# Optimization experiments

Hardware: AMD Instinct MI355X
Metric: run time of the kernel (lower is better)

Reference implementation:

```python
import jax, jax.numpy as jnp
import numpy as np

N = 100000                       # all_nodes_num
COUNTS = (40000, 30000, 30000)   # node_type_split_list; type 0 is the attributed type
HID = 64                         # args.hidden_dim
K = 8                            # args.cluster_num
E = 1_600_000                    # number of edges in g
D_IN = 512                       # in_dims[valid_attributed_type]
NCLS = 16                        # num_classes


def _spmm_mean(h, src, dst):
    """Degree-normalized sparse adjacency @ h via gather/segment_sum (edge-list spmm)."""
    deg = jax.ops.segment_sum(jnp.ones_like(src, dtype=h.dtype), dst, num_segments=N)
    agg = jax.ops.segment_sum(h[src], dst, num_segments=N)  # [N, HID]
    return agg / jnp.maximum(deg, 1.0)[:, None]


def setup_inputs() -> dict:
    key = jax.random.key(0)
    ks = jax.random.split(key, 16)
    s = lambda k, shp, fan: jax.random.normal(k, shp, jnp.float32) * np.float32(1.0 / np.sqrt(fan))
    return {
        "feats0": jax.random.normal(ks[0], (COUNTS[0], D_IN), jnp.float32),
        "W_pre": s(ks[1], (D_IN, HID), D_IN), "b_pre": jnp.zeros((HID,), jnp.float32),
        "emb_W": s(ks[2], (2, COUNTS[1], HID), COUNTS[1]), "emb_b": jnp.zeros((2, HID), jnp.float32),
        "op_W": s(ks[3], (K, HID, HID), HID), "op_b": jnp.zeros((K, HID), jnp.float32),
        "fc_W": s(ks[4], (2, HID, HID), HID), "fc_b": jnp.zeros((2, HID), jnp.float32),
        "gnn_W": s(ks[5], (HID, HID), HID), "gnn_b": jnp.zeros((HID,), jnp.float32),
        "out_W": s(ks[6], (HID, NCLS), HID), "out_b": jnp.zeros((NCLS,), jnp.float32),
        "src": jax.random.randint(ks[7], (E,), 0, N, jnp.int32),
        "dst": jax.random.randint(ks[8], (E,), 0, N, jnp.int32),
        "node_assign": jax.random.randint(ks[9], (N,), 0, K, jnp.int32),
    }


def reference(feats0, W_pre, b_pre, emb_W, emb_b, op_W, op_b, fc_W, fc_b,
              gnn_W, gnn_b, out_W, out_b, src, dst, node_assign):
    # preprocess: Linear on the attributed type, scattered into h0 over all nodes
    h_attr = feats0 @ W_pre + b_pre                       # [n0, HID]
    h0 = jnp.zeros((N, HID), feats0.dtype).at[:COUNTS[0]].set(h_attr)

    # 'one-hot' embeddings: Linear applied to sparse identity == weight rows + bias
    one_hot_h = jnp.concatenate([
        jnp.zeros((COUNTS[0], HID), feats0.dtype),
        emb_W[0] + emb_b[0],
        emb_W[1] + emb_b[1],
    ], axis=0)                                            # [N, HID]

    # shared heterogeneous-graph aggregation (edge-list spmm), per-cluster op linear,
    # then diagonal cluster mask (spmm with diagonal selection matrix == row masking)
    agg = _spmm_mean(h0, src, dst)                        # [N, HID]
    h_att = h0
    for k in range(K):
        mask = (node_assign == k)[:, None]
        gcn_k = agg @ op_W[k] + op_b[k]                   # per-cluster GNN op output
        h_att = h_att + jnp.where(mask, gcn_k + one_hot_h, 0.0)

    # useTypeLinear: per-type Linear for non-attributed types, identity for attributed
    parts = [h_att[:COUNTS[0]]]
    off = COUNTS[0]
    for i in range(2):
        seg = h_att[off:off + COUNTS[1 + i]]
        parts.append(seg @ fc_W[i] + fc_b[i])
        off += COUNTS[1 + i]
    h_t = jnp.concatenate(parts, axis=0)                  # [N, HID]

    # downstream GCN-style model: spmm -> linear -> elu, then classifier head
    node_emb = jax.nn.elu(_spmm_mean(h_t, src, dst) @ gnn_W + gnn_b)
    logits = node_emb @ out_W + out_b
    return node_emb, logits, logits
```

## Files before the change

### kernel.cpp

```cpp
#include <hip/hip_runtime.h>
#include <hip/hip_bf16.h>

#define NN   100000
#define C0   40000
#define C1   30000
#define C2   30000
#define HID  64
#define KK   8
#define EE   1600000
#define DIN  512
#define NCLS 16
#define NB   196
#define BKE  2048
#define GR1  782
#define NBC  1568
#define MAXT 1571
#define FCT  469
#define GNT  1563
#define AP   88

typedef unsigned short ushortT;
typedef __attribute__((ext_vector_type(8))) short bf16x8;
typedef __attribute__((ext_vector_type(4))) float f32x4;

__device__ __forceinline__ float b2f(ushortT u) {
    return __uint_as_float((unsigned)u << 16);
}
__device__ __forceinline__ ushortT f2b(float x) {
    unsigned v = __float_as_uint(x);
    unsigned r = (v + 0x7FFF + ((v >> 16) & 1)) >> 16;
    return (ushortT)r;
}
__device__ __forceinline__ unsigned pk2(float lo, float hi) {
    return (unsigned)f2b(lo) | ((unsigned)f2b(hi) << 16);
}
__device__ __forceinline__ void acc8f(float* a, uint4 v) {
    a[0] += b2f((ushortT)(v.x & 0xFFFF)); a[1] += b2f((ushortT)(v.x >> 16));
    a[2] += b2f((ushortT)(v.y & 0xFFFF)); a[3] += b2f((ushortT)(v.y >> 16));
    a[4] += b2f((ushortT)(v.z & 0xFFFF)); a[5] += b2f((ushortT)(v.z >> 16));
    a[6] += b2f((ushortT)(v.w & 0xFFFF)); a[7] += b2f((ushortT)(v.w >> 16));
}

__global__ __launch_bounds__(256) void setup_k(const int* __restrict__ dst,
                                               const int* __restrict__ na,
                                               const float* __restrict__ W,
                                               int* __restrict__ bcnt,
                                               int* __restrict__ nbc,
                                               ushortT* __restrict__ WT) {
    __shared__ int sh[NB];
    const int t = threadIdx.x, b = blockIdx.x;
    if (b < GR1) {
        for (int i = t; i < NB; i += 256) sh[i] = 0;
        __syncthreads();
        const int base = b * BKE;
        for (int u = 0; u < BKE / 256; ++u) {
            int e = base + t + u * 256;
            if (e < EE) atomicAdd(&sh[dst[e] >> 9], 1);
        }
        __syncthreads();
        for (int i = t; i < NB; i += 256) {
            int c = sh[i];
            if (c) atomicAdd(&bcnt[i], c);
        }
    } else if (b < GR1 + NB) {
        const int nb_ = b - GR1;
        if (t < KK) sh[t] = 0;
        __syncthreads();
        #pragma unroll
        for (int u = 0; u < 2; ++u) {
            int n = nb_ * 512 + t + u * 256;
            if (n < NN) atomicAdd(&sh[na[n]], 1);
        }
        __syncthreads();
        if (t < KK) nbc[t * NB + nb_] = sh[t];
    } else {
        int idx = (b - GR1 - NB) * 256 + t;
        int c = idx >> 6, k8 = (idx & 63) * 8;
        uint4 v;
        v.x = pk2(W[(size_t)(k8 + 0) * HID + c], W[(size_t)(k8 + 1) * HID + c]);
        v.y = pk2(W[(size_t)(k8 + 2) * HID + c], W[(size_t)(k8 + 3) * HID + c]);
        v.z = pk2(W[(size_t)(k8 + 4) * HID + c], W[(size_t)(k8 + 5) * HID + c]);
        v.w = pk2(W[(size_t)(k8 + 6) * HID + c], W[(size_t)(k8 + 7) * HID + c]);
        *(uint4*)(WT + (size_t)c * DIN + k8) = v;
    }
}

__global__ __launch_bounds__(256) void pre_mfma(const float* __restrict__ A,
                                                const ushortT* __restrict__ WT,
                                                const float* __restrict__ b,
                                                ushortT* __restrict__ hb) {
    __shared__ ushortT Ak[2][64 * AP];
    __shared__ ushortT Bk[2][64 * AP];
    const int tid = threadIdx.x;
    const int row0 = blockIdx.x * 64;
    const int rr = tid >> 2, q = tid & 3;
    const int w = tid >> 6, l = tid & 63;
    const int lr = l & 15, g = l >> 4;
    f32x4 acc[4] = {{0.f,0.f,0.f,0.f},{0.f,0.f,0.f,0.f},{0.f,0.f,0.f,0.f},{0.f,0.f,0.f,0.f}};
    float4 av0, av1, av2, av3;
    uint4 bv0, bv1;
    {
        const float* ap = A + (size_t)(row0 + rr) * DIN + q * 16;
        av0 = *(const float4*)(ap + 0);  av1 = *(const float4*)(ap + 4);
        av2 = *(const float4*)(ap + 8);  av3 = *(const float4*)(ap + 12);
        const uint4* bp = (const uint4*)(WT + (size_t)rr * DIN + q * 16);
        bv0 = bp[0]; bv1 = bp[1];
    }
    {
        uint4 ua0, ua1;
        ua0.x = pk2(av0.x, av0.y); ua0.y = pk2(av0.z, av0.w);
        ua0.z = pk2(av1.x, av1.y); ua0.w = pk2(av1.z, av1.w);
        ua1.x = pk2(av2.x, av2.y); ua1.y = pk2(av2.z, av2.w);
        ua1.z = pk2(av3.x, av3.y); ua1.w = pk2(av3.z, av3.w);
        *(uint4*)&Ak[0][rr * AP + q * 16] = ua0;
        *(uint4*)&Ak[0][rr * AP + q * 16 + 8] = ua1;
        *(uint4*)&Bk[0][rr * AP + q * 16] = bv0;
        *(uint4*)&Bk[0][rr * AP + q * 16 + 8] = bv1;
    }
    __syncthreads();
    for (int t = 0; t < 8; ++t) {
        if (t < 7) {
            const int k0 = (t + 1) * 64;
            const float* ap = A + (size_t)(row0 + rr) * DIN + k0 + q * 16;
            av0 = *(const float4*)(ap + 0);  av1 = *(const float4*)(ap + 4);
            av2 = *(const float4*)(ap + 8);  av3 = *(const float4*)(ap + 12);
            const uint4* bp = (const uint4*)(WT + (size_t)rr * DIN + k0 + q * 16);
            bv0 = bp[0]; bv1 = bp[1];
        }
        const int bu = t & 1;
        #pragma unroll
        for (int s = 0; s < 2; ++s) {
            bf16x8 af = *(const bf16x8*)&Ak[bu][(w * 16 + lr) * AP + s * 32 + g * 8];
            #pragma unroll
            for (int n = 0; n < 4; ++n) {
                bf16x8 bf = *(const bf16x8*)&Bk[bu][(n * 16 + lr) * AP + s * 32 + g * 8];
                acc[n] = __builtin_amdgcn_mfma_f32_16x16x32_bf16(af, bf, acc[n], 0, 0, 0);
            }
        }
        if (t < 7) {
            const int nb = (t + 1) & 1;
            uint4 ua0, ua1;
            ua0.x = pk2(av0.x, av0.y); ua0.y = pk2(av0.z, av0.w);
            ua0.z = pk2(av1.x, av1.y); ua0.w = pk2(av1.z, av1.w);
            ua1.x = pk2(av2.x, av2.y); ua1.y = pk2(av2.z, av2.w);
            ua1.z = pk2(av3.x, av3.y); ua1.w = pk2(av3.z, av3.w);
            *(uint4*)&Ak[nb][rr * AP + q * 16] = ua0;
            *(uint4*)&Ak[nb][rr * AP + q * 16 + 8] = ua1;
            *(uint4*)&Bk[nb][rr * AP + q * 16] = bv0;
            *(uint4*)&Bk[nb][rr * AP + q * 16 + 8] = bv1;
        }
        __syncthreads();
    }
    #pragma unroll
    for (int n = 0; n < 4; ++n) {
        float bb = b[n * 16 + lr];
        #pragma unroll
        for (int i = 0; i < 4; ++i) {
            int row = row0 + w * 16 + g * 4 + i;
            hb[(size_t)row * HID + n * 16 + lr] = f2b(acc[n][i] + bb);
        }
    }
}

__global__ __launch_bounds__(256) void scan_k(const int* __restrict__ bcnt,
                                              int* __restrict__ bbase,
                                              int* __restrict__ bcur,
                                              int* __restrict__ offs,
                                              const int* __restrict__ nbc,
                                              int* __restrict__ gbase,
                                              int* __restrict__ koff,
                                              int* __restrict__ tmap_b,
                                              int* __restrict__ tmap_s) {
    const int t = threadIdx.x;
    if (blockIdx.x == 0) {
        if (t == 0) {
            int run = 0;
            for (int i = 0; i < NB; ++i) { bbase[i] = run; bcur[i] = run; run += bcnt[i]; }
            offs[NN] = EE;
        }
        return;
    }
    __shared__ int sm[256];
    __shared__ int carry;
    __shared__ int tl[KK];
    if (t == 0) carry = 0;
    for (int i = t; i < MAXT; i += 256) tmap_b[i] = -1;
    __syncthreads();
    for (int c = 0; c < 7; ++c) {
        int i = c * 256 + t;
        int v = (i < NBC) ? nbc[i] : 0;
        sm[t] = v;
        __syncthreads();
        for (int off = 1; off < 256; off <<= 1) {
            int y = (t >= off) ? sm[t - off] : 0;
            __syncthreads();
            sm[t] += y;
            __syncthreads();
        }
        int base = carry;
        int excl = base + sm[t] - v;
        if (i < NBC) {
            gbase[i] = excl;
            if ((i % NB) == 0) koff[i / NB] = excl;
        }
        __syncthreads();
        if (t == 255) carry = base + sm[255];
        __syncthreads();
    }
    if (t == 0) {
        koff[KK] = NN;
        int run = 0;
        for (int k = 0; k < KK; ++k) {
            tl[k] = run;
            int cnt = ((k == KK - 1) ? NN : koff[k + 1]) - koff[k];
            run += (cnt + 63) / 64;
        }
    }
    __syncthreads();
    if (t < KK) {
        int k = t;
        int kb = koff[k];
        int ke = (k == KK - 1) ? NN : koff[k + 1];
        int nt = (ke - kb + 63) / 64;
        for (int tt = 0; tt < nt; ++tt) {
            tmap_b[tl[k] + tt] = k;
            tmap_s[tl[k] + tt] = kb + tt * 64;
        }
    }
}

__global__ __launch_bounds__(256) void scatter_k(const int* __restrict__ src,
                                                 const int* __restrict__ dst,
                                                 int* __restrict__ bcur,
                                                 unsigned* __restrict__ ebuf,
                                                 const int* __restrict__ na,
                                                 const int* __restrict__ gbase,
                                                 int* __restrict__ perm) {
    __shared__ int s1[NB];
    __shared__ int s2[NB];
    const int t = threadIdx.x, b = blockIdx.x;
    if (b < GR1) {
        for (int i = t; i < NB; i += 256) s1[i] = 0;
        __syncthreads();
        const int base = b * BKE;
        unsigned mypk[8]; int mybin[8], myrank[8];
        #pragma unroll
        for (int u = 0; u < 8; ++u) {
            int e = base + t + u * 256;
            if (e < EE) {
                int d = dst[e];
                int s = src[e];
                mybin[u] = d >> 9;
                mypk[u] = (unsigned)s |
                          ((unsigned)(((d & 511) << 1) | (s < C0 ? 0 : 1)) << 17);
                myrank[u] = atomicAdd(&s1[mybin[u]], 1);
            } else mybin[u] = -1;
        }
        __syncthreads();
        for (int i = t; i < NB; i += 256) {
            int c = s1[i];
            s2[i] = c ? atomicAdd(&bcur[i], c) : 0;
        }
        __syncthreads();
        #pragma unroll
        for (int u = 0; u < 8; ++u) {
            if (mybin[u] >= 0) {
                ebuf[s2[mybin[u]] + myrank[u]] = mypk[u];
            }
        }
    } else {
        const int nb_ = b - GR1;
        if (t < KK) { s1[t] = 0; s2[t] = gbase[t * NB + nb_]; }
        __syncthreads();
        #pragma unroll
        for (int u = 0; u < 2; ++u) {
            int n = nb_ * 512 + t + u * 256;
            if (n < NN) {
                int k = na[n];
                int r = atomicAdd(&s1[k], 1);
                perm[s2[k] + r] = n;
            }
        }
    }
}

__global__ __launch_bounds__(256) void fine_scatter(const unsigned* __restrict__ ebuf,
                                                    const int* __restrict__ bbase,
                                                    const int* __restrict__ bend,
                                                    int* __restrict__ offs,
                                                    int* __restrict__ split,
                                                    int* __restrict__ ssrc) {
    __shared__ int hist[1024];
    __shared__ int lofs[1024];
    __shared__ int sm[256];
    const int t = threadIdx.x, b = blockIdx.x;
    const int beg = bbase[b], end = bend[b];
    for (int i = t; i < 1024; i += 256) hist[i] = 0;
    __syncthreads();
    for (int j = beg + t; j < end; j += 256) {
        unsigned pk = ebuf[j];
        atomicAdd(&hist[pk >> 17], 1);
    }
    __syncthreads();
    int v0 = hist[4 * t], v1 = hist[4 * t + 1], v2 = hist[4 * t + 2], v3 = hist[4 * t + 3];
    int ts = v0 + v1 + v2 + v3;
    sm[t] = ts;
    __syncthreads();
    for (int off = 1; off < 256; off <<= 1) {
        int y = (t >= off) ? sm[t - off] : 0;
        __syncthreads();
        sm[t] += y;
        __syncthreads();
    }
    int pre = sm[t] - ts;
    lofs[4 * t] = pre; lofs[4 * t + 1] = pre + v0;
    lofs[4 * t + 2] = pre + v0 + v1; lofs[4 * t + 3] = pre + v0 + v1 + v2;
    __syncthreads();
    const int d0 = b * 512;
    for (int i = t; i < 512; i += 256) {
        int n = d0 + i;
        if (n < NN) {
            offs[n]  = beg + lofs[2 * i];
            split[n] = beg + lofs[2 * i + 1];
        }
    }
    __syncthreads();
    for (int j = beg + t; j < end; j += 256) {
        unsigned pk = ebuf[j];
        int pos = beg + atomicAdd(&lofs[pk >> 17], 1);
        ssrc[pos] = (int)(pk & 0x1FFFFu);
    }
}

__global__ __launch_bounds__(256) void spmm(const ushortT* __restrict__ rows,
                                            const int* __restrict__ offs,
                                            const int* __restrict__ splt,
                                            const int* __restrict__ ssrc,
                                            ushortT* __restrict__ aggb) {
    const int t = threadIdx.x;
    const int g = t >> 3, c8 = t & 7;
    const int n = blockIdx.x * 32 + g;
    const int beg = offs[n], endf = offs[n + 1];
    const int ge = splt ? splt[n] : endf;
    float a[8] = {}, c[8] = {};
    int j = beg;
    for (; j + 8 <= ge; j += 8) {
        int s0 = ssrc[j + 0], s1 = ssrc[j + 1], s2 = ssrc[j + 2], s3 = ssrc[j + 3];
        int s4 = ssrc[j + 4], s5 = ssrc[j + 5], s6 = ssrc[j + 6], s7 = ssrc[j + 7];
        uint4 v0 = *(const uint4*)(rows + (size_t)s0 * HID + c8 * 8);
        uint4 v1 = *(const uint4*)(rows + (size_t)s1 * HID + c8 * 8);
        uint4 v2 = *(const uint4*)(rows + (size_t)s2 * HID + c8 * 8);
        uint4 v3 = *(const uint4*)(rows + (size_t)s3 * HID + c8 * 8);
        uint4 v4 = *(const uint4*)(rows + (size_t)s4 * HID + c8 * 8);
        uint4 v5 = *(const uint4*)(rows + (size_t)s5 * HID + c8 * 8);
        uint4 v6 = *(const uint4*)(rows + (size_t)s6 * HID + c8 * 8);
        uint4 v7 = *(const uint4*)(rows + (size_t)s7 * HID + c8 * 8);
        acc8f(a, v0); acc8f(c, v1); acc8f(a, v2); acc8f(c, v3);
        acc8f(a, v4); acc8f(c, v5); acc8f(a, v6); acc8f(c, v7);
    }
    if (j + 4 <= ge) {
        int s0 = ssrc[j + 0], s1 = ssrc[j + 1], s2 = ssrc[j + 2], s3 = ssrc[j + 3];
        uint4 v0 = *(const uint4*)(rows + (size_t)s0 * HID + c8 * 8);
        uint4 v1 = *(const uint4*)(rows + (size_t)s1 * HID + c8 * 8);
        uint4 v2 = *(const uint4*)(rows + (size_t)s2 * HID + c8 * 8);
        uint4 v3 = *(const uint4*)(rows + (size_t)s3 * HID + c8 * 8);
        acc8f(a, v0); acc8f(c, v1); acc8f(a, v2); acc8f(c, v3);
        j += 4;
    }
    for (; j < ge; ++j) {
        uint4 v = *(const uint4*)(rows + (size_t)ssrc[j] * HID + c8 * 8);
        acc8f(a, v);
    }
    const float inv = 1.0f / fmaxf((float)(endf - beg), 1.0f);
    #pragma unroll
    for (int i = 0; i < 8; ++i) a[i] = (a[i] + c[i]) * inv;
    uint4 o;
    o.x = pk2(a[0], a[1]); o.y = pk2(a[2], a[3]);
    o.z = pk2(a[4], a[5]); o.w = pk2(a[6], a[7]);
    *(uint4*)(aggb + (size_t)n * HID + c8 * 8) = o;
}

__device__ __forceinline__ void gemm64(const float As[64][65], const float Bs[64][64],
                                       float acc[4][4], int tx, int ty) {
    for (int kk = 0; kk < 64; ++kk) {
        float a0 = As[ty * 4 + 0][kk], a1 = As[ty * 4 + 1][kk];
        float a2 = As[ty * 4 + 2][kk], a3 = As[ty * 4 + 3][kk];
        float4 bv = *(const float4*)(&Bs[kk][tx * 4]);
        acc[0][0] += a0 * bv.x; acc[0][1] += a0 * bv.y; acc[0][2] += a0 * bv.z; acc[0][3] += a0 * bv.w;
        acc[1][0] += a1 * bv.x; acc[1][1] += a1 * bv.y; acc[1][2] += a1 * bv.z; acc[1][3] += a1 * bv.w;
        acc[2][0] += a2 * bv.x; acc[2][1] += a2 * bv.y; acc[2][2] += a2 * bv.z; acc[2][3] += a2 * bv.w;
        acc[3][0] += a3 * bv.x; acc[3][1] += a3 * bv.y; acc[3][2] += a3 * bv.z; acc[3][3] += a3 * bv.w;
    }
}

__global__ __launch_bounds__(256) void op_gemm(const ushortT* __restrict__ aggb,
                                               const ushortT* __restrict__ hb,
                                               const int* __restrict__ perm,
                                               const int* __restrict__ koff,
                                               const int* __restrict__ tmap_b,
                                               const int* __restrict__ tmap_s,
                                               const float* __restrict__ op_W,
                                               const float* __restrict__ op_b,
                                               const float* __restrict__ emb_W,
                                               const float* __restrict__ emb_b,
                                               ushortT* __restrict__ htb) {
    __shared__ float As[64][65];
    __shared__ float Bs[64][64];
    __shared__ int idx[64];
    const int bk = tmap_b[blockIdx.x];
    if (bk < 0) return;
    const int start = tmap_s[blockIdx.x];
    const int kend = koff[bk + 1];
    const int tid = threadIdx.x;
    if (tid < 64) {
        int p = start + tid;
        idx[tid] = (p < kend) ? perm[p] : -1;
    }
    __syncthreads();
    for (int i = tid; i < 64 * 16; i += 256) {
        int r = i >> 4, c4 = i & 15;
        int n = idx[r];
        if (n >= 0) {
            ushort4 u = *(const ushort4*)(aggb + (size_t)n * HID + c4 * 4);
            As[r][c4 * 4 + 0] = b2f(u.x); As[r][c4 * 4 + 1] = b2f(u.y);
            As[r][c4 * 4 + 2] = b2f(u.z); As[r][c4 * 4 + 3] = b2f(u.w);
        } else {
            As[r][c4 * 4 + 0] = 0.f; As[r][c4 * 4 + 1] = 0.f;
            As[r][c4 * 4 + 2] = 0.f; As[r][c4 * 4 + 3] = 0.f;
        }
    }
    for (int i = tid; i < 64 * 16; i += 256) {
        int r = i >> 4, c4 = i & 15;
        *(float4*)(&Bs[r][c4 * 4]) = *(const float4*)(op_W + (size_t)bk * HID * HID + (size_t)r * HID + c4 * 4);
    }
    __syncthreads();
    const int tx = tid & 15, ty = tid >> 4;
    float acc[4][4] = {};
    gemm64(As, Bs, acc, tx, ty);
    float4 ob = *(const float4*)(op_b + (size_t)bk * HID + tx * 4);
    #pragma unroll
    for (int rr = 0; rr < 4; ++rr) {
        int n = idx[ty * 4 + rr];
        if (n < 0) continue;
        float4 v;
        v.x = acc[rr][0] + ob.x; v.y = acc[rr][1] + ob.y;
        v.z = acc[rr][2] + ob.z; v.w = acc[rr][3] + ob.w;
        if (n < C0) {
            ushort4 hu = *(const ushort4*)(hb + (size_t)n * HID + tx * 4);
            v.x += b2f(hu.x); v.y += b2f(hu.y); v.z += b2f(hu.z); v.w += b2f(hu.w);
        } else {
            int si = (n < C0 + C1) ? 0 : 1;
            int rn = n - C0 - si * C1;
            float4 ew = *(const float4*)(emb_W + ((size_t)si * C1 + rn) * HID + tx * 4);
            float4 eb = *(const float4*)(emb_b + (size_t)si * HID + tx * 4);
            v.x += ew.x + eb.x; v.y += ew.y + eb.y;
            v.z += ew.z + eb.z; v.w += ew.w + eb.w;
        }
        ushort4 o;
        o.x = f2b(v.x); o.y = f2b(v.y); o.z = f2b(v.z); o.w = f2b(v.w);
        *(ushort4*)(htb + (size_t)n * HID + tx * 4) = o;
    }
}

__global__ __launch_bounds__(256) void fc_gemm(ushortT* __restrict__ htb,
                                               const float* __restrict__ fc_W,
                                               const float* __restrict__ fc_b) {
    __shared__ float As[64][65];
    __shared__ float Bs[64][64];
    const int si = (blockIdx.x < FCT) ? 0 : 1;
    const int t0 = blockIdx.x - si * FCT;
    const int row0 = C0 + si * C1 + t0 * 64;
    const int lim = C0 + (si + 1) * C1;
    const int tid = threadIdx.x;
    for (int i = tid; i < 64 * 16; i += 256) {
        int r = i >> 4, c4 = i & 15;
        int n = row0 + r;
        if (n < lim) {
            ushort4 u = *(const ushort4*)(htb + (size_t)n * HID + c4 * 4);
            As[r][c4 * 4 + 0] = b2f(u.x); As[r][c4 * 4 + 1] = b2f(u.y);
            As[r][c4 * 4 + 2] = b2f(u.z); As[r][c4 * 4 + 3] = b2f(u.w);
        } else {
            As[r][c4 * 4 + 0] = 0.f; As[r][c4 * 4 + 1] = 0.f;
            As[r][c4 * 4 + 2] = 0.f; As[r][c4 * 4 + 3] = 0.f;
        }
    }
    for (int i = tid; i < 64 * 16; i += 256) {
        int r = i >> 4, c4 = i & 15;
        *(float4*)(&Bs[r][c4 * 4]) = *(const float4*)(fc_W + (size_t)si * HID * HID + (size_t)r * HID + c4 * 4);
    }
    __syncthreads();
    const int tx = tid & 15, ty = tid >> 4;
    float acc[4][4] = {};
    gemm64(As, Bs, acc, tx, ty);
    float4 fb = *(const float4*)(fc_b + (size_t)si * HID + tx * 4);
    #pragma unroll
    for (int rr = 0; rr < 4; ++rr) {
        int n = row0 + ty * 4 + rr;
        if (n >= lim) continue;
        ushort4 o;
        o.x = f2b(acc[rr][0] + fb.x); o.y = f2b(acc[rr][1] + fb.y);
        o.z = f2b(acc[rr][2] + fb.z); o.w = f2b(acc[rr][3] + fb.w);
        *(ushort4*)(htb + (size_t)n * HID + tx * 4) = o;
    }
}

__global__ __launch_bounds__(256) void gnn_logits(const ushortT* __restrict__ aggb,
                                                  const float* __restrict__ gnn_W,
                                                  const float* __restrict__ gnn_b,
                                                  const float* __restrict__ out_W,
                                                  const float* __restrict__ out_b,
                                                  float* __restrict__ out) {
    __shared__ float As[64][65];
    __shared__ float Bs[64][64];
    __shared__ float Wo[64 * NCLS];
    const int row0 = blockIdx.x * 64;
    const int tid = threadIdx.x;
    for (int i = tid; i < 64 * 16; i += 256) {
        int r = i >> 4, c4 = i & 15;
        int n = row0 + r;
        if (n < NN) {
            ushort4 u = *(const ushort4*)(aggb + (size_t)n * HID + c4 * 4);
            As[r][c4 * 4 + 0] = b2f(u.x); As[r][c4 * 4 + 1] = b2f(u.y);
            As[r][c4 * 4 + 2] = b2f(u.z); As[r][c4 * 4 + 3] = b2f(u.w);
        } else {
            As[r][c4 * 4 + 0] = 0.f; As[r][c4 * 4 + 1] = 0.f;
            As[r][c4 * 4 + 2] = 0.f; As[r][c4 * 4 + 3] = 0.f;
        }
    }
    for (int i = tid; i < 64 * 16; i += 256) {
        int r = i >> 4, c4 = i & 15;
        *(float4*)(&Bs[r][c4 * 4]) = *(const float4*)(gnn_W + (size_t)r * HID + c4 * 4);
    }
    *(float4*)(&Wo[tid * 4]) = *(const float4*)(out_W + tid * 4);
    __syncthreads();
    const int tx = tid & 15, ty = tid >> 4;
    float acc[4][4] = {};
    gemm64(As, Bs, acc, tx, ty);
    __syncthreads();
    float4 gb = *(const float4*)(gnn_b + tx * 4);
    #pragma unroll
    for (int rr = 0; rr < 4; ++rr) {
        int n = row0 + ty * 4 + rr;
        float4 v;
        v.x = acc[rr][0] + gb.x; v.y = acc[rr][1] + gb.y;
        v.z = acc[rr][2] + gb.z; v.w = acc[rr][3] + gb.w;
        v.x = (v.x > 0.f) ? v.x : expm1f(v.x);
        v.y = (v.y > 0.f) ? v.y : expm1f(v.y);
        v.z = (v.z > 0.f) ? v.z : expm1f(v.z);
        v.w = (v.w > 0.f) ? v.w : expm1f(v.w);
        As[ty * 4 + rr][tx * 4 + 0] = v.x; As[ty * 4 + rr][tx * 4 + 1] = v.y;
        As[ty * 4 + rr][tx * 4 + 2] = v.z; As[ty * 4 + rr][tx * 4 + 3] = v.w;
        if (n < NN) *(float4*)(out + (size_t)n * HID + tx * 4) = v;
    }
    __syncthreads();
    const int r = tid >> 2, cq = (tid & 3) * 4;
    float l0 = 0.f, l1 = 0.f, l2 = 0.f, l3 = 0.f;
    #pragma unroll 8
    for (int j = 0; j < 64; ++j) {
        float e = As[r][j];
        float4 w = *(const float4*)(&Wo[j * NCLS + cq]);
        l0 += e * w.x; l1 += e * w.y; l2 += e * w.z; l3 += e * w.w;
    }
    int n = row0 + r;
    if (n < NN) {
        float4 ob = *(const float4*)(out_b + cq);
        float4 lg;
        lg.x = l0 + ob.x; lg.y = l1 + ob.y; lg.z = l2 + ob.z; lg.w = l3 + ob.w;
        const size_t lbase = (size_t)NN * HID;
        *(float4*)(out + lbase + (size_t)n * NCLS + cq) = lg;
        *(float4*)(out + lbase + (size_t)NN * NCLS + (size_t)n * NCLS + cq) = lg;
    }
}

extern "C" void kernel_launch(void* const* d_in, const int* in_sizes, int n_in,
                              void* d_out, int out_size, void* d_ws, size_t ws_size,
                              hipStream_t stream) {
    const float* feats0 = (const float*)d_in[0];
    const float* W_pre  = (const float*)d_in[1];
    const float* b_pre  = (const float*)d_in[2];
    const float* emb_W  = (const float*)d_in[3];
    const float* emb_b  = (const float*)d_in[4];
    const float* op_W   = (const float*)d_in[5];
    const float* op_b   = (const float*)d_in[6];
    const float* fc_W   = (const float*)d_in[7];
    const float* fc_b   = (const float*)d_in[8];
    const float* gnn_W  = (const float*)d_in[9];
    const float* gnn_b  = (const float*)d_in[10];
    const float* out_W  = (const float*)d_in[11];
    const float* out_b  = (const float*)d_in[12];
    const int* src         = (const int*)d_in[13];
    const int* dst         = (const int*)d_in[14];
    const int* node_assign = (const int*)d_in[15];
    float* out = (float*)d_out;

    ushortT* hb  = (ushortT*)d_ws;
    ushortT* htb = hb + (size_t)C0 * HID;
    ushortT* aggb = htb + (size_t)NN * HID;
    unsigned* ebuf = (unsigned*)aggb;
    ushortT* WT = aggb + (size_t)NN * HID;
    int* ssrc   = (int*)(WT + (size_t)HID * DIN);
    int* offs   = ssrc + EE;
    int* split  = offs + NN + 1;
    int* perm   = split + NN;
    int* nbc    = perm + NN;
    int* gbase  = nbc + NBC;
    int* koff   = gbase + NBC;
    int* tmap_b = koff + KK + 1;
    int* tmap_s = tmap_b + MAXT;
    int* bcnt   = tmap_s + MAXT;
    int* bbase  = bcnt + NB;
    int* bcur   = bbase + NB;

    hipMemsetAsync(bcnt, 0, NB * sizeof(int), stream);

    setup_k<<<GR1 + NB + 16, 256, 0, stream>>>(dst, node_assign, W_pre, bcnt, nbc, WT);
    pre_mfma<<<C0 / 64, 256, 0, stream>>>(feats0, WT, b_pre, hb);
    scan_k<<<2, 256, 0, stream>>>(bcnt, bbase, bcur, offs, nbc, gbase, koff, tmap_b, tmap_s);
    scatter_k<<<GR1 + NB, 256, 0, stream>>>(src, dst, bcur, ebuf, node_assign, gbase, perm);
    fine_scatter<<<NB, 256, 0, stream>>>(ebuf, bbase, bcur, offs, split, ssrc);
    spmm<<<NN / 32, 256, 0, stream>>>(hb, offs, split, ssrc, aggb);
    op_gemm<<<MAXT, 256, 0, stream>>>(aggb, hb, perm, koff, tmap_b, tmap_s,
                                      op_W, op_b, emb_W, emb_b, htb);
    fc_gemm<<<2 * FCT, 256, 0, stream>>>(htb, fc_W, fc_b);
    spmm<<<NN / 32, 256, 0, stream>>>(htb, offs, nullptr, ssrc, aggb);
    gnn_logits<<<GNT, 256, 0, stream>>>(aggb, gnn_W, gnn_b, out_W, out_b, out);
}
```

Baseline: 223.2 us.

## Fuse per-type fc linear into cluster op GEMM via type-by-cluster binning

Nodes are now binned by (node type, cluster) into 24 bins instead of 8 clusters, so every 64-row tile in op_gemm holds a single type. For non-attributed types the op GEMM result plus embedding is staged in shared memory and immediately multiplied by the per-type fc weight, which removes the separate fc_gemm kernel and its round-trip of htb through global memory. The bucket-offset scan is also parallelised from a serial single-thread loop to a block scan. In exchange the node scan grows from 7 to 19 chunks, there are more partially filled tiles, and some blocks do a second GEMM.

```diff
diff --git a/kernel.cpp b/kernel.cpp
--- a/kernel.cpp
+++ b/kernel.cpp
@@ -13,9 +13,10 @@
 #define NB   196
 #define BKE  2048
 #define GR1  782
-#define NBC  1568
-#define MAXT 1571
-#define FCT  469
+#define NBS  24
+#define NBC  (NBS*NB)
+#define SCH  19
+#define MAXT 1600
 #define GNT  1563
 #define AP   88
 
@@ -39,6 +40,9 @@
     a[2] += b2f((ushortT)(v.y & 0xFFFF)); a[3] += b2f((ushortT)(v.y >> 16));
     a[4] += b2f((ushortT)(v.z & 0xFFFF)); a[5] += b2f((ushortT)(v.z >> 16));
     a[6] += b2f((ushortT)(v.w & 0xFFFF)); a[7] += b2f((ushortT)(v.w >> 16));
+}
+__device__ __forceinline__ int seg_of(int n) {
+    return (n < C0) ? 0 : ((n < C0 + C1) ? 1 : 2);
 }
 
 __global__ __launch_bounds__(256) void setup_k(const int* __restrict__ dst,
@@ -64,15 +68,15 @@
         }
     } else if (b < GR1 + NB) {
         const int nb_ = b - GR1;
-        if (t < KK) sh[t] = 0;
+        if (t < NBS) sh[t] = 0;
         __syncthreads();
         #pragma unroll
         for (int u = 0; u < 2; ++u) {
             int n = nb_ * 512 + t + u * 256;
-            if (n < NN) atomicAdd(&sh[na[n]], 1);
-        }
-        __syncthreads();
-        if (t < KK) nbc[t * NB + nb_] = sh[t];
+            if (n < NN) atomicAdd(&sh[seg_of(n) * KK + na[n]], 1);
+        }
+        __syncthreads();
+        if (t < NBS) nbc[t * NB + nb_] = sh[t];
     } else {
         int idx = (b - GR1 - NB) * 256 + t;
         int c = idx >> 6, k8 = (idx & 63) * 8;
@@ -171,24 +175,10 @@
                                               int* __restrict__ koff,
                                               int* __restrict__ tmap_b,
                                               int* __restrict__ tmap_s) {
+    __shared__ int sm[256];
     const int t = threadIdx.x;
     if (blockIdx.x == 0) {
-        if (t == 0) {
-            int run = 0;
-            for (int i = 0; i < NB; ++i) { bbase[i] = run; bcur[i] = run; run += bcnt[i]; }
-            offs[NN] = EE;
-        }
-        return;
-    }
-    __shared__ int sm[256];
-    __shared__ int carry;
-    __shared__ int tl[KK];
-    if (t == 0) carry = 0;
-    for (int i = t; i < MAXT; i += 256) tmap_b[i] = -1;
-    __syncthreads();
-    for (int c = 0; c < 7; ++c) {
-        int i = c * 256 + t;
-        int v = (i < NBC) ? nbc[i] : 0;
+        int v = (t < NB) ? bcnt[t] : 0;
         sm[t] = v;
         __syncthreads();
         for (int off = 1; off < 256; off <<= 1) {
@@ -197,6 +187,30 @@
             sm[t] += y;
             __syncthreads();
         }
+        if (t < NB) {
+            int excl = sm[t] - v;
+            bbase[t] = excl;
+            bcur[t] = excl;
+        }
+        if (t == 0) offs[NN] = EE;
+        return;
+    }
+    __shared__ int carry;
+    __shared__ int tl[NBS];
+    if (t == 0) carry = 0;
+    for (int i = t; i < MAXT; i += 256) tmap_b[i] = -1;
+    __syncthreads();
+    for (int c = 0; c < SCH; ++c) {
+        int i = c * 256 + t;
+        int v = (i < NBC) ? nbc[i] : 0;
+        sm[t] = v;
+        __syncthreads();
+        for (int off = 1; off < 256; off <<= 1) {
+            int y = (t >= off) ? sm[t - off] : 0;
+            __syncthreads();
+            sm[t] += y;
+            __syncthreads();
+        }
         int base = carry;
         int excl = base + sm[t] - v;
         if (i < NBC) {
@@ -208,19 +222,19 @@
         __syncthreads();
     }
     if (t == 0) {
-        koff[KK] = NN;
+        koff[NBS] = NN;
         int run = 0;
-        for (int k = 0; k < KK; ++k) {
+        for (int k = 0; k < NBS; ++k) {
             tl[k] = run;
-            int cnt = ((k == KK - 1) ? NN : koff[k + 1]) - koff[k];
+            int cnt = ((k == NBS - 1) ? NN : koff[k + 1]) - koff[k];
             run += (cnt + 63) / 64;
         }
     }
     __syncthreads();
-    if (t < KK) {
+    if (t < NBS) {
         int k = t;
         int kb = koff[k];
-        int ke = (k == KK - 1) ? NN : koff[k + 1];
+        int ke = (k == NBS - 1) ? NN : koff[k + 1];
         int nt = (ke - kb + 63) / 64;
         for (int tt = 0; tt < nt; ++tt) {
             tmap_b[tl[k] + tt] = k;
@@ -270,15 +284,15 @@
         }
     } else {
         const int nb_ = b - GR1;
-        if (t < KK) { s1[t] = 0; s2[t] = gbase[t * NB + nb_]; }
+        if (t < NBS) { s1[t] = 0; s2[t] = gbase[t * NB + nb_]; }
         __syncthreads();
         #pragma unroll
         for (int u = 0; u < 2; ++u) {
             int n = nb_ * 512 + t + u * 256;
             if (n < NN) {
-                int k = na[n];
-                int r = atomicAdd(&s1[k], 1);
-                perm[s2[k] + r] = n;
+                int bin = seg_of(n) * KK + na[n];
+                int r = atomicAdd(&s1[bin], 1);
+                perm[s2[bin] + r] = n;
             }
         }
     }
@@ -403,14 +417,18 @@
                                                const float* __restrict__ op_b,
                                                const float* __restrict__ emb_W,
                                                const float* __restrict__ emb_b,
+                                               const float* __restrict__ fc_W,
+                                               const float* __restrict__ fc_b,
                                                ushortT* __restrict__ htb) {
     __shared__ float As[64][65];
     __shared__ float Bs[64][64];
     __shared__ int idx[64];
-    const int bk = tmap_b[blockIdx.x];
-    if (bk < 0) return;
+    const int bin = tmap_b[blockIdx.x];
+    if (bin < 0) return;
+    const int bk = bin & 7;
+    const int si = bin >> 3;
     const int start = tmap_s[blockIdx.x];
-    const int kend = koff[bk + 1];
+    const int kend = koff[bin + 1];
     const int tid = threadIdx.x;
     if (tid < 64) {
         int p = start + tid;
@@ -438,69 +456,54 @@
     float acc[4][4] = {};
     gemm64(As, Bs, acc, tx, ty);
     float4 ob = *(const float4*)(op_b + (size_t)bk * HID + tx * 4);
-    #pragma unroll
-    for (int rr = 0; rr < 4; ++rr) {
-        int n = idx[ty * 4 + rr];
-        if (n < 0) continue;
-        float4 v;
-        v.x = acc[rr][0] + ob.x; v.y = acc[rr][1] + ob.y;
-        v.z = acc[rr][2] + ob.z; v.w = acc[rr][3] + ob.w;
-        if (n < C0) {
+    if (si == 0) {
+        #pragma unroll
+        for (int rr = 0; rr < 4; ++rr) {
+            int n = idx[ty * 4 + rr];
+            if (n < 0) continue;
             ushort4 hu = *(const ushort4*)(hb + (size_t)n * HID + tx * 4);
-            v.x += b2f(hu.x); v.y += b2f(hu.y); v.z += b2f(hu.z); v.w += b2f(hu.w);
-        } else {
-            int si = (n < C0 + C1) ? 0 : 1;
-            int rn = n - C0 - si * C1;
-            float4 ew = *(const float4*)(emb_W + ((size_t)si * C1 + rn) * HID + tx * 4);
-            float4 eb = *(const float4*)(emb_b + (size_t)si * HID + tx * 4);
-            v.x += ew.x + eb.x; v.y += ew.y + eb.y;
-            v.z += ew.z + eb.z; v.w += ew.w + eb.w;
-        }
-        ushort4 o;
-        o.x = f2b(v.x); o.y = f2b(v.y); o.z = f2b(v.z); o.w = f2b(v.w);
-        *(ushort4*)(htb + (size_t)n * HID + tx * 4) = o;
-    }
-}
-
-__global__ __launch_bounds__(256) void fc_gemm(ushortT* __restrict__ htb,
-                                               const float* __restrict__ fc_W,
-                                               const float* __restrict__ fc_b) {
-    __shared__ float As[64][65];
-    __shared__ float Bs[64][64];
-    const int si = (blockIdx.x < FCT) ? 0 : 1;
-    const int t0 = blockIdx.x - si * FCT;
-    const int row0 = C0 + si * C1 + t0 * 64;
-    const int lim = C0 + (si + 1) * C1;
-    const int tid = threadIdx.x;
-    for (int i = tid; i < 64 * 16; i += 256) {
-        int r = i >> 4, c4 = i & 15;
-        int n = row0 + r;
-        if (n < lim) {
-            ushort4 u = *(const ushort4*)(htb + (size_t)n * HID + c4 * 4);
-            As[r][c4 * 4 + 0] = b2f(u.x); As[r][c4 * 4 + 1] = b2f(u.y);
-            As[r][c4 * 4 + 2] = b2f(u.z); As[r][c4 * 4 + 3] = b2f(u.w);
-        } else {
-            As[r][c4 * 4 + 0] = 0.f; As[r][c4 * 4 + 1] = 0.f;
-            As[r][c4 * 4 + 2] = 0.f; As[r][c4 * 4 + 3] = 0.f;
-        }
-    }
-    for (int i = tid; i < 64 * 16; i += 256) {
-        int r = i >> 4, c4 = i & 15;
-        *(float4*)(&Bs[r][c4 * 4]) = *(const float4*)(fc_W + (size_t)si * HID * HID + (size_t)r * HID + c4 * 4);
-    }
-    __syncthreads();
-    const int tx = tid & 15, ty = tid >> 4;
-    float acc[4][4] = {};
-    gemm64(As, Bs, acc, tx, ty);
-    float4 fb = *(const float4*)(fc_b + (size_t)si * HID + tx * 4);
-    #pragma unroll
-    for (int rr = 0; rr < 4; ++rr) {
-        int n = row0 + ty * 4 + rr;
-        if (n >= lim) continue;
-        ushort4 o;
-        o.x = f2b(acc[rr][0] + fb.x); o.y = f2b(acc[rr][1] + fb.y);
-        o.z = f2b(acc[rr][2] + fb.z); o.w = f2b(acc[rr][3] + fb.w);
-        *(ushort4*)(htb + (size_t)n * HID + tx * 4) = o;
+            ushort4 o;
+            o.x = f2b(acc[rr][0] + ob.x + b2f(hu.x));
+            o.y = f2b(acc[rr][1] + ob.y + b2f(hu.y));
+            o.z = f2b(acc[rr][2] + ob.z + b2f(hu.z));
+            o.w = f2b(acc[rr][3] + ob.w + b2f(hu.w));
+            *(ushort4*)(htb + (size_t)n * HID + tx * 4) = o;
+        }
+    } else {
+        const int ei = si - 1;
+        float4 eb = *(const float4*)(emb_b + (size_t)ei * HID + tx * 4);
+        __syncthreads();
+        #pragma unroll
+        for (int rr = 0; rr < 4; ++rr) {
+            int n = idx[ty * 4 + rr];
+            float4 v;
+            v.x = acc[rr][0] + ob.x + eb.x; v.y = acc[rr][1] + ob.y + eb.y;
+            v.z = acc[rr][2] + ob.z + eb.z; v.w = acc[rr][3] + ob.w + eb.w;
+            if (n >= 0) {
+                int rn = n - C0 - ei * C1;
+                float4 ew = *(const float4*)(emb_W + ((size_t)ei * C1 + rn) * HID + tx * 4);
+                v.x += ew.x; v.y += ew.y; v.z += ew.z; v.w += ew.w;
+            }
+            As[ty * 4 + rr][tx * 4 + 0] = v.x; As[ty * 4 + rr][tx * 4 + 1] = v.y;
+            As[ty * 4 + rr][tx * 4 + 2] = v.z; As[ty * 4 + rr][tx * 4 + 3] = v.w;
+        }
+        for (int i = tid; i < 64 * 16; i += 256) {
+            int r = i >> 4, c4 = i & 15;
+            *(float4*)(&Bs[r][c4 * 4]) = *(const float4*)(fc_W + (size_t)ei * HID * HID + (size_t)r * HID + c4 * 4);
+        }
+        __syncthreads();
+        float acc2[4][4] = {};
+        gemm64(As, Bs, acc2, tx, ty);
+        float4 fb = *(const float4*)(fc_b + (size_t)ei * HID + tx * 4);
+        #pragma unroll
+        for (int rr = 0; rr < 4; ++rr) {
+            int n = idx[ty * 4 + rr];
+            if (n < 0) continue;
+            ushort4 o;
+            o.x = f2b(acc2[rr][0] + fb.x); o.y = f2b(acc2[rr][1] + fb.y);
+            o.z = f2b(acc2[rr][2] + fb.z); o.w = f2b(acc2[rr][3] + fb.w);
+            *(ushort4*)(htb + (size_t)n * HID + tx * 4) = o;
+        }
     }
 }
 
@@ -605,7 +608,7 @@
     int* nbc    = perm + NN;
     int* gbase  = nbc + NBC;
     int* koff   = gbase + NBC;
-    int* tmap_b = koff + KK + 1;
+    int* tmap_b = koff + NBS + 1;
     int* tmap_s = tmap_b + MAXT;
     int* bcnt   = tmap_s + MAXT;
     int* bbase  = bcnt + NB;
@@ -620,8 +623,7 @@
     fine_scatter<<<NB, 256, 0, stream>>>(ebuf, bbase, bcur, offs, split, ssrc);
     spmm<<<NN / 32, 256, 0, stream>>>(hb, offs, split, ssrc, aggb);
     op_gemm<<<MAXT, 256, 0, stream>>>(aggb, hb, perm, koff, tmap_b, tmap_s,
-                                      op_W, op_b, emb_W, emb_b, htb);
-    fc_gemm<<<2 * FCT, 256, 0, stream>>>(htb, fc_W, fc_b);
+                                      op_W, op_b, emb_W, emb_b, fc_W, fc_b, htb);
     spmm<<<NN / 32, 256, 0, stream>>>(htb, offs, nullptr, ssrc, aggb);
     gnn_logits<<<GNT, 256, 0, stream>>>(aggb, gnn_W, gnn_b, out_W, out_b, out);
 }
```

New measurement: 238.6 us. 1.07x slower.

## Fuse histogram setup into the pre-linear MFMA kernel and parallelize bucket scan

Applied to the files above, without the earlier changes.

Moves the dst-bucket histogram and per-cluster node counts out of the setup kernel and into the same launch as the preprocessing MFMA GEMM, as extra blocks that reuse its LDS. A small kernel now does the weight transpose and zeroes the bucket counters, replacing the memset. The serial single-thread bucket prefix sum becomes a 256-thread parallel scan. The goal is to cut launch overhead and let the atomic-heavy histogram overlap with the GEMM, at the cost of mixing heterogeneous blocks in one grid.

```diff
diff --git a/kernel.cpp b/kernel.cpp
--- a/kernel.cpp
+++ b/kernel.cpp
@@ -13,7 +13,9 @@
 #define NB   196
 #define BKE  2048
 #define GR1  782
+#define PMB  625
 #define NBC  1568
+#define SCH  7
 #define MAXT 1571
 #define FCT  469
 #define GNT  1563
@@ -41,40 +43,12 @@
     a[6] += b2f((ushortT)(v.w & 0xFFFF)); a[7] += b2f((ushortT)(v.w >> 16));
 }
 
-__global__ __launch_bounds__(256) void setup_k(const int* __restrict__ dst,
-                                               const int* __restrict__ na,
-                                               const float* __restrict__ W,
-                                               int* __restrict__ bcnt,
-                                               int* __restrict__ nbc,
-                                               ushortT* __restrict__ WT) {
-    __shared__ int sh[NB];
+__global__ __launch_bounds__(256) void zero_wt(const float* __restrict__ W,
+                                               ushortT* __restrict__ WT,
+                                               int* __restrict__ bcnt) {
     const int t = threadIdx.x, b = blockIdx.x;
-    if (b < GR1) {
-        for (int i = t; i < NB; i += 256) sh[i] = 0;
-        __syncthreads();
-        const int base = b * BKE;
-        for (int u = 0; u < BKE / 256; ++u) {
-            int e = base + t + u * 256;
-            if (e < EE) atomicAdd(&sh[dst[e] >> 9], 1);
-        }
-        __syncthreads();
-        for (int i = t; i < NB; i += 256) {
-            int c = sh[i];
-            if (c) atomicAdd(&bcnt[i], c);
-        }
-    } else if (b < GR1 + NB) {
-        const int nb_ = b - GR1;
-        if (t < KK) sh[t] = 0;
-        __syncthreads();
-        #pragma unroll
-        for (int u = 0; u < 2; ++u) {
-            int n = nb_ * 512 + t + u * 256;
-            if (n < NN) atomicAdd(&sh[na[n]], 1);
-        }
-        __syncthreads();
-        if (t < KK) nbc[t * NB + nb_] = sh[t];
-    } else {
-        int idx = (b - GR1 - NB) * 256 + t;
+    if (b < 16) {
+        int idx = b * 256 + t;
         int c = idx >> 6, k8 = (idx & 63) * 8;
         uint4 v;
         v.x = pk2(W[(size_t)(k8 + 0) * HID + c], W[(size_t)(k8 + 1) * HID + c]);
@@ -82,83 +56,117 @@
         v.z = pk2(W[(size_t)(k8 + 4) * HID + c], W[(size_t)(k8 + 5) * HID + c]);
         v.w = pk2(W[(size_t)(k8 + 6) * HID + c], W[(size_t)(k8 + 7) * HID + c]);
         *(uint4*)(WT + (size_t)c * DIN + k8) = v;
-    }
-}
-
-__global__ __launch_bounds__(256) void pre_mfma(const float* __restrict__ A,
-                                                const ushortT* __restrict__ WT,
-                                                const float* __restrict__ b,
-                                                ushortT* __restrict__ hb) {
+    } else {
+        if (t < NB) bcnt[t] = 0;
+    }
+}
+
+__global__ __launch_bounds__(256) void fused_a(const float* __restrict__ A,
+                                               const ushortT* __restrict__ WT,
+                                               const float* __restrict__ bias,
+                                               const int* __restrict__ dst,
+                                               const int* __restrict__ na,
+                                               int* __restrict__ bcnt,
+                                               int* __restrict__ nbc,
+                                               ushortT* __restrict__ hb) {
     __shared__ ushortT Ak[2][64 * AP];
     __shared__ ushortT Bk[2][64 * AP];
-    const int tid = threadIdx.x;
-    const int row0 = blockIdx.x * 64;
-    const int rr = tid >> 2, q = tid & 3;
-    const int w = tid >> 6, l = tid & 63;
-    const int lr = l & 15, g = l >> 4;
-    f32x4 acc[4] = {{0.f,0.f,0.f,0.f},{0.f,0.f,0.f,0.f},{0.f,0.f,0.f,0.f},{0.f,0.f,0.f,0.f}};
-    float4 av0, av1, av2, av3;
-    uint4 bv0, bv1;
-    {
-        const float* ap = A + (size_t)(row0 + rr) * DIN + q * 16;
-        av0 = *(const float4*)(ap + 0);  av1 = *(const float4*)(ap + 4);
-        av2 = *(const float4*)(ap + 8);  av3 = *(const float4*)(ap + 12);
-        const uint4* bp = (const uint4*)(WT + (size_t)rr * DIN + q * 16);
-        bv0 = bp[0]; bv1 = bp[1];
-    }
-    {
-        uint4 ua0, ua1;
-        ua0.x = pk2(av0.x, av0.y); ua0.y = pk2(av0.z, av0.w);
-        ua0.z = pk2(av1.x, av1.y); ua0.w = pk2(av1.z, av1.w);
-        ua1.x = pk2(av2.x, av2.y); ua1.y = pk2(av2.z, av2.w);
-        ua1.z = pk2(av3.x, av3.y); ua1.w = pk2(av3.z, av3.w);
-        *(uint4*)&Ak[0][rr * AP + q * 16] = ua0;
-        *(uint4*)&Ak[0][rr * AP + q * 16 + 8] = ua1;
-        *(uint4*)&Bk[0][rr * AP + q * 16] = bv0;
-        *(uint4*)&Bk[0][rr * AP + q * 16 + 8] = bv1;
-    }
-    __syncthreads();
-    for (int t = 0; t < 8; ++t) {
-        if (t < 7) {
-            const int k0 = (t + 1) * 64;
-            const float* ap = A + (size_t)(row0 + rr) * DIN + k0 + q * 16;
+    const int tid = threadIdx.x, b = blockIdx.x;
+    if (b < PMB) {
+        const int row0 = b * 64;
+        const int rr = tid >> 2, q = tid & 3;
+        const int w = tid >> 6, l = tid & 63;
+        const int lr = l & 15, g = l >> 4;
+        f32x4 acc[4] = {{0.f,0.f,0.f,0.f},{0.f,0.f,0.f,0.f},{0.f,0.f,0.f,0.f},{0.f,0.f,0.f,0.f}};
+        float4 av0, av1, av2, av3;
+        uint4 bv0, bv1;
+        {
+            const float* ap = A + (size_t)(row0 + rr) * DIN + q * 16;
             av0 = *(const float4*)(ap + 0);  av1 = *(const float4*)(ap + 4);
             av2 = *(const float4*)(ap + 8);  av3 = *(const float4*)(ap + 12);
-            const uint4* bp = (const uint4*)(WT + (size_t)rr * DIN + k0 + q * 16);
+            const uint4* bp = (const uint4*)(WT + (size_t)rr * DIN + q * 16);
             bv0 = bp[0]; bv1 = bp[1];
         }
-        const int bu = t & 1;
-        #pragma unroll
-        for (int s = 0; s < 2; ++s) {
-            bf16x8 af = *(const bf16x8*)&Ak[bu][(w * 16 + lr) * AP + s * 32 + g * 8];
-            #pragma unroll
-            for (int n = 0; n < 4; ++n) {
-                bf16x8 bf = *(const bf16x8*)&Bk[bu][(n * 16 + lr) * AP + s * 32 + g * 8];
-                acc[n] = __builtin_amdgcn_mfma_f32_16x16x32_bf16(af, bf, acc[n], 0, 0, 0);
-            }
-        }
-        if (t < 7) {
-            const int nb = (t + 1) & 1;
+        {
             uint4 ua0, ua1;
             ua0.x = pk2(av0.x, av0.y); ua0.y = pk2(av0.z, av0.w);
             ua0.z = pk2(av1.x, av1.y); ua0.w = pk2(av1.z, av1.w);
             ua1.x = pk2(av2.x, av2.y); ua1.y = pk2(av2.z, av2.w);
             ua1.z = pk2(av3.x, av3.y); ua1.w = pk2(av3.z, av3.w);
-            *(uint4*)&Ak[nb][rr * AP + q * 16] = ua0;
-            *(uint4*)&Ak[nb][rr * AP + q * 16 + 8] = ua1;
-            *(uint4*)&Bk[nb][rr * AP + q * 16] = bv0;
-            *(uint4*)&Bk[nb][rr * AP + q * 16 + 8] = bv1;
-        }
-        __syncthreads();
-    }
-    #pragma unroll
-    for (int n = 0; n < 4; ++n) {
-        float bb = b[n * 16 + lr];
+            *(uint4*)&Ak[0][rr * AP + q * 16] = ua0;
+            *(uint4*)&Ak[0][rr * AP + q * 16 + 8] = ua1;
+            *(uint4*)&Bk[0][rr * AP + q * 16] = bv0;
+            *(uint4*)&Bk[0][rr * AP + q * 16 + 8] = bv1;
+        }
+        __syncthreads();
+        for (int tt = 0; tt < 8; ++tt) {
+            if (tt < 7) {
+                const int k0 = (tt + 1) * 64;
+                const float* ap = A + (size_t)(row0 + rr) * DIN + k0 + q * 16;
+                av0 = *(const float4*)(ap + 0);  av1 = *(const float4*)(ap + 4);
+                av2 = *(const float4*)(ap + 8);  av3 = *(const float4*)(ap + 12);
+                const uint4* bp = (const uint4*)(WT + (size_t)rr * DIN + k0 + q * 16);
+                bv0 = bp[0]; bv1 = bp[1];
+            }
+            const int bu = tt & 1;
+            #pragma unroll
+            for (int s = 0; s < 2; ++s) {
+                bf16x8 af = *(const bf16x8*)&Ak[bu][(w * 16 + lr) * AP + s * 32 + g * 8];
+                #pragma unroll
+                for (int n = 0; n < 4; ++n) {
+                    bf16x8 bf = *(const bf16x8*)&Bk[bu][(n * 16 + lr) * AP + s * 32 + g * 8];
+                    acc[n] = __builtin_amdgcn_mfma_f32_16x16x32_bf16(af, bf, acc[n], 0, 0, 0);
+                }
+            }
+            if (tt < 7) {
+                const int nb2 = (tt + 1) & 1;
+                uint4 ua0, ua1;
+                ua0.x = pk2(av0.x, av0.y); ua0.y = pk2(av0.z, av0.w);
+                ua0.z = pk2(av1.x, av1.y); ua0.w = pk2(av1.z, av1.w);
+                ua1.x = pk2(av2.x, av2.y); ua1.y = pk2(av2.z, av2.w);
+                ua1.z = pk2(av3.x, av3.y); ua1.w = pk2(av3.z, av3.w);
+                *(uint4*)&Ak[nb2][rr * AP + q * 16] = ua0;
+                *(uint4*)&Ak[nb2][rr * AP + q * 16 + 8] = ua1;
+                *(uint4*)&Bk[nb2][rr * AP + q * 16] = bv0;
+                *(uint4*)&Bk[nb2][rr * AP + q * 16 + 8] = bv1;
+            }
+            __syncthreads();
+        }
         #pragma unroll
-        for (int i = 0; i < 4; ++i) {
-            int row = row0 + w * 16 + g * 4 + i;
-            hb[(size_t)row * HID + n * 16 + lr] = f2b(acc[n][i] + bb);
-        }
+        for (int n = 0; n < 4; ++n) {
+            float bb = bias[n * 16 + lr];
+            #pragma unroll
+            for (int i = 0; i < 4; ++i) {
+                int row = row0 + w * 16 + g * 4 + i;
+                hb[(size_t)row * HID + n * 16 + lr] = f2b(acc[n][i] + bb);
+            }
+        }
+    } else if (b < PMB + GR1) {
+        int* sh = (int*)&Ak[0][0];
+        for (int i = tid; i < NB; i += 256) sh[i] = 0;
+        __syncthreads();
+        const int base = (b - PMB) * BKE;
+        for (int u = 0; u < BKE / 256; ++u) {
+            int e = base + tid + u * 256;
+            if (e < EE) atomicAdd(&sh[dst[e] >> 9], 1);
+        }
+        __syncthreads();
+        for (int i = tid; i < NB; i += 256) {
+            int c = sh[i];
+            if (c) atomicAdd(&bcnt[i], c);
+        }
+    } else {
+        int* sh = (int*)&Ak[0][0];
+        const int nb_ = b - PMB - GR1;
+        if (tid < KK) sh[tid] = 0;
+        __syncthreads();
+        #pragma unroll
+        for (int u = 0; u < 2; ++u) {
+            int n = nb_ * 512 + tid + u * 256;
+            if (n < NN) atomicAdd(&sh[na[n]], 1);
+        }
+        __syncthreads();
+        if (tid < KK) nbc[tid * NB + nb_] = sh[tid];
     }
 }
 
@@ -171,22 +179,32 @@
                                               int* __restrict__ koff,
                                               int* __restrict__ tmap_b,
                                               int* __restrict__ tmap_s) {
+    __shared__ int sm[256];
     const int t = threadIdx.x;
     if (blockIdx.x == 0) {
-        if (t == 0) {
-            int run = 0;
-            for (int i = 0; i < NB; ++i) { bbase[i] = run; bcur[i] = run; run += bcnt[i]; }
-            offs[NN] = EE;
-        }
+        int v = (t < NB) ? bcnt[t] : 0;
+        sm[t] = v;
+        __syncthreads();
+        for (int off = 1; off < 256; off <<= 1) {
+            int y = (t >= off) ? sm[t - off] : 0;
+            __syncthreads();
+            sm[t] += y;
+            __syncthreads();
+        }
+        if (t < NB) {
+            int excl = sm[t] - v;
+            bbase[t] = excl;
+            bcur[t] = excl;
+        }
+        if (t == 0) offs[NN] = EE;
         return;
     }
-    __shared__ int sm[256];
     __shared__ int carry;
     __shared__ int tl[KK];
     if (t == 0) carry = 0;
     for (int i = t; i < MAXT; i += 256) tmap_b[i] = -1;
     __syncthreads();
-    for (int c = 0; c < 7; ++c) {
+    for (int c = 0; c < SCH; ++c) {
         int i = c * 256 + t;
         int v = (i < NBC) ? nbc[i] : 0;
         sm[t] = v;
@@ -611,10 +629,9 @@
     int* bbase  = bcnt + NB;
     int* bcur   = bbase + NB;
 
-    hipMemsetAsync(bcnt, 0, NB * sizeof(int), stream);
-
-    setup_k<<<GR1 + NB + 16, 256, 0, stream>>>(dst, node_assign, W_pre, bcnt, nbc, WT);
-    pre_mfma<<<C0 / 64, 256, 0, stream>>>(feats0, WT, b_pre, hb);
+    zero_wt<<<17, 256, 0, stream>>>(W_pre, WT, bcnt);
+    fused_a<<<PMB + GR1 + NB, 256, 0, stream>>>(feats0, WT, b_pre, dst, node_assign,
+                                                bcnt, nbc, hb);
     scan_k<<<2, 256, 0, stream>>>(bcnt, bbase, bcur, offs, nbc, gbase, koff, tmap_b, tmap_s);
     scatter_k<<<GR1 + NB, 256, 0, stream>>>(src, dst, bcur, ebuf, node_assign, gbase, perm);
     fine_scatter<<<NB, 256, 0, stream>>>(ebuf, bbase, bcur, offs, split, ssrc);
```

Measured after the change: 213.1 us. -4.5%, faster.
